# Performance work log

Measured on AMD Instinct MI355X. Metric: run time of the kernel, lower is better.

## Reference

```python
import jax, jax.numpy as jnp
import numpy as np

N_NODES = 50000


def gcn_conv(x, W, b, src, dst, num_nodes):
    """PyG GCNConv: add self-loops, symmetric deg^{-1/2} normalization,
    linear transform, scatter-add aggregation, bias."""
    loop = jnp.arange(num_nodes, dtype=src.dtype)
    s = jnp.concatenate([src, loop])  # message sources
    d = jnp.concatenate([dst, loop])  # message destinations
    deg = jax.ops.segment_sum(jnp.ones_like(d, dtype=x.dtype), d, num_segments=num_nodes)
    dinv = jnp.where(deg > 0, jax.lax.rsqrt(deg), 0.0)
    norm = dinv[s] * dinv[d]                      # [E+N]
    h = x @ W                                      # [N, out]
    msg = h[s] * norm[:, None]                     # gather + scale  [E+N, out]
    out = jax.ops.segment_sum(msg, d, num_segments=num_nodes)  # scatter-add
    return out + b


def setup_inputs() -> dict:
    key = jax.random.key(0)
    ks = jax.random.split(key, 8)
    n, e = N_NODES, 1600000
    d_in, d_h, d_out = 128, 128, 64
    x = jax.random.normal(ks[0], (n, d_in), dtype=jnp.float32)
    edge_index = jax.random.randint(ks[1], (2, e), 0, n, dtype=jnp.int32)
    s = 1.0 / np.sqrt(d_in)
    W1 = jax.random.uniform(ks[2], (d_in, d_h), jnp.float32, -s, s)
    b1 = jnp.zeros((d_h,), jnp.float32)
    W2 = jax.random.uniform(ks[3], (d_h, d_h), jnp.float32, -s, s)
    b2 = jnp.zeros((d_h,), jnp.float32)
    W3 = jax.random.uniform(ks[4], (d_h, d_out), jnp.float32, -s, s)
    b3 = jnp.zeros((d_out,), jnp.float32)
    return {"x": x, "edge_index": edge_index, "W1": W1, "b1": b1,
            "W2": W2, "b2": b2, "W3": W3, "b3": b3}


def reference(x, edge_index, W1, b1, W2, b2, W3, b3):
    src, dst = edge_index[0], edge_index[1]
    n = x.shape[0]
    # Dropout in eval mode (identity); ReLU between GCN layers.
    h = jax.nn.relu(gcn_conv(x, W1, b1, src, dst, n))
    h = jax.nn.relu(gcn_conv(h, W2, b2, src, dst, n))
    out = gcn_conv(h, W3, b3, src, dst, n)
    return out
```

## Files before the change

### kernel.cpp

```cpp
#include <hip/hip_runtime.h>
#include <type_traits>


#define EPB  4096
#define DIRW 197

typedef __attribute__((ext_vector_type(8))) short bf16x8;
typedef __attribute__((ext_vector_type(4))) float f32x4;
typedef __attribute__((ext_vector_type(2))) float f32x2;

__device__ __forceinline__ unsigned short f2bf(float f) {
    unsigned int u = __float_as_uint(f);
    u += 0x7FFFu + ((u >> 16) & 1u);
    return (unsigned short)(u >> 16);
}
__device__ __forceinline__ float bflo(unsigned int u) { return __uint_as_float(u << 16); }
__device__ __forceinline__ float bfhi(unsigned int u) { return __uint_as_float(u & 0xFFFF0000u); }

__global__ __launch_bounds__(256) void bin_wtrans_kernel(const int* __restrict__ src,
                                                         const int* __restrict__ dst,
                                                         unsigned int* __restrict__ pair_buf,
                                                         int* __restrict__ dir,
                                                         int E, int nbkt, int NB,
                                                         const float* __restrict__ W1,
                                                         const float* __restrict__ W2,
                                                         const float* __restrict__ W3,
                                                         unsigned short* __restrict__ Wt1,
                                                         unsigned short* __restrict__ Wt2,
                                                         unsigned short* __restrict__ Wt3,
                                                         unsigned int* __restrict__ hb_pad_row) {
    int blk = blockIdx.x;
    if (blk >= NB) {
        int wb = blk - NB;
        const float* W; unsigned short* Wt; int N, e0;
        if (wb < 64)       { W = W1; Wt = Wt1; N = 128; e0 = wb * 256; }
        else if (wb < 128) { W = W2; Wt = Wt2; N = 128; e0 = (wb - 64) * 256; }
        else               { W = W3; Wt = Wt3; N = 64;  e0 = (wb - 128) * 256; }
        int e = e0 + threadIdx.x;
        int nn = e >> 7, k = e & 127;
        Wt[e] = f2bf(W[(size_t)k * N + nn]);
        if (wb == 0 && threadIdx.x < 32) hb_pad_row[threadIdx.x] = 0u;
        return;
    }
    __shared__ unsigned int stage[EPB];
    __shared__ int hist[DIRW];
    __shared__ int sc[256];
    __shared__ int cur[DIRW];
    int tid = threadIdx.x;
    if (tid < DIRW) hist[tid] = 0;
    __syncthreads();

    int s_reg[16], d_reg[16];
#pragma unroll
    for (int j = 0; j < 16; ++j) {
        int gi = blk * EPB + j * 256 + tid;
        int s = 0, d = nbkt << 8;
        if (gi < E) { s = src[gi]; d = dst[gi]; }
        s_reg[j] = s; d_reg[j] = d;
        atomicAdd(&hist[d >> 8], 1);
    }
    __syncthreads();
    int h = (tid < DIRW) ? hist[tid] : 0;
    sc[tid] = h;
    __syncthreads();
#pragma unroll
    for (int off = 1; off < 256; off <<= 1) {
        int v = (tid >= off) ? sc[tid - off] : 0;
        __syncthreads();
        sc[tid] += v;
        __syncthreads();
    }
    if (tid < DIRW) {
        int st = sc[tid] - h;
        cur[tid] = st;
        dir[blk * DIRW + tid] = st;
    }
    __syncthreads();
#pragma unroll
    for (int j = 0; j < 16; ++j) {
        int b = d_reg[j] >> 8;
        int slot = atomicAdd(&cur[b], 1);
        stage[slot] = ((unsigned int)s_reg[j] << 8) | (unsigned int)(d_reg[j] & 255);
    }
    __syncthreads();
#pragma unroll
    for (int j = 0; j < 16; ++j) {
        int idx = j * 256 + tid;
        pair_buf[blk * EPB + idx] = stage[idx];
    }
}

__global__ __launch_bounds__(512) void csr_sizes_kernel(const unsigned int* __restrict__ pair_buf,
                                                        const int* __restrict__ dir,
                                                        int* __restrict__ bucket_pad,
                                                        int* __restrict__ node_cnt,
                                                        float* __restrict__ dinv,
                                                        int NB, int n) {
    __shared__ int dstart[400];
    __shared__ int dend[400];
    __shared__ int cnt[256];
    int tid = threadIdx.x;
    int b = blockIdx.x;
    for (int i = tid; i < NB; i += 512) {
        dstart[i] = dir[i * DIRW + b];
        dend[i]   = dir[i * DIRW + b + 1];
    }
    if (tid < 256) cnt[tid] = 0;
    __syncthreads();
    int wid = tid >> 6, lane = tid & 63;
    for (int seg = wid; seg < NB; seg += 8) {
        int s0 = dstart[seg], s1 = dend[seg];
        for (int k = s0 + lane; k < s1; k += 64) {
            unsigned int p = pair_buf[(size_t)seg * EPB + k];
            atomicAdd(&cnt[p & 255u], 1);
        }
    }
    __syncthreads();
    if (tid < 256) {
        node_cnt[b * 256 + tid] = cnt[tid];
        int d = b * 256 + tid;
        if (d < n) dinv[d] = rsqrtf((float)(cnt[tid] + 1));
    }
    if (tid < 64) {
        int m = max(max(cnt[4 * tid], cnt[4 * tid + 1]),
                    max(cnt[4 * tid + 2], cnt[4 * tid + 3]));
        int L = (m + 7) & ~7;
        int s = L;
#pragma unroll
        for (int off = 1; off < 64; off <<= 1) s += __shfl_xor(s, off);
        if (tid == 0) bucket_pad[b] = 4 * s;
    }
}

__global__ __launch_bounds__(512) void csr_place_kernel(const unsigned int* __restrict__ pair_buf,
                                                        const int* __restrict__ dir,
                                                        const int* __restrict__ bucket_pad,
                                                        const int* __restrict__ node_cnt,
                                                        int* __restrict__ row_ptr,
                                                        unsigned short* __restrict__ csr_src,
                                                        int n, int NB, int nbkt) {
    __shared__ int dstart[400];
    __shared__ int dend[400];
    __shared__ int psc[256];
    __shared__ int Lg[64];
    __shared__ int Lpre[64];
    __shared__ int nbase[256];
    __shared__ int cur[256];
    __shared__ int cend[256];
    int tid = threadIdx.x;
    int b = blockIdx.x;
    for (int i = tid; i < NB; i += 512) {
        dstart[i] = dir[i * DIRW + b];
        dend[i]   = dir[i * DIRW + b + 1];
    }
    if (tid < 256) psc[tid] = (tid < nbkt) ? bucket_pad[tid] : 0;
    __syncthreads();
#pragma unroll
    for (int off = 1; off < 256; off <<= 1) {
        int v = 0;
        if (tid < 256 && tid >= off) v = psc[tid - off];
        __syncthreads();
        if (tid < 256) psc[tid] += v;
        __syncthreads();
    }
    int base = (b > 0) ? psc[b - 1] : 0;
    if (b == nbkt - 1 && tid == 0) row_ptr[n] = psc[nbkt - 1];
    if (tid < 64) {
        int c0 = node_cnt[b * 256 + 4 * tid + 0];
        int c1 = node_cnt[b * 256 + 4 * tid + 1];
        int c2 = node_cnt[b * 256 + 4 * tid + 2];
        int c3 = node_cnt[b * 256 + 4 * tid + 3];
        int m = max(max(c0, c1), max(c2, c3));
        int L = (m + 7) & ~7;
        int x = L;
#pragma unroll
        for (int off = 1; off < 64; off <<= 1) {
            int y = __shfl_up(x, off);
            if (tid >= off) x += y;
        }
        Lg[tid] = L;
        Lpre[tid] = x - L;
    }
    __syncthreads();
    if (tid < 256) {
        int g = tid >> 2;
        int nb = base + 4 * Lpre[g] + (tid & 3) * Lg[g];
        nbase[tid] = nb;
        cur[tid] = nb;
        cend[tid] = nb + Lg[g];
        int d = b * 256 + tid;
        if (d < n) row_ptr[d] = nb;
    }
    __syncthreads();
    int wid = tid >> 6, lane = tid & 63;
    for (int seg = wid; seg < NB; seg += 8) {
        int s0 = dstart[seg], s1 = dend[seg];
        for (int k = s0 + lane; k < s1; k += 64) {
            unsigned int p = pair_buf[(size_t)seg * EPB + k];
            int pos = atomicAdd(&cur[p & 255u], 1);
            csr_src[pos] = (unsigned short)(p >> 8);
        }
    }
    __syncthreads();
    if (tid < 256) {
        for (int pos = cur[tid]; pos < cend[tid]; ++pos)
            csr_src[pos] = (unsigned short)n;
    }
}

template <int NOUT, typename TA, bool FP8OUT>
__global__ __launch_bounds__(256) void gemm_bf16_kernel(const TA* __restrict__ X,
                                                        const unsigned short* __restrict__ Wt,
                                                        const float* __restrict__ dinv,
                                                        void* __restrict__ Hout,
                                                        int n_rows) {
    __shared__ short As[64][136];
    __shared__ short Bs[NOUT][136];
    int tid = threadIdx.x;
    int row0 = blockIdx.x * 64;

    {
        int r = tid >> 2;
        int c0 = (tid & 3) * 32;
        int grow = row0 + r;
        if constexpr (std::is_same<TA, float>::value) {
            const float* xp = X + (size_t)grow * 128 + c0;
#pragma unroll
            for (int j = 0; j < 8; ++j) {
                float4 v = (grow < n_rows) ? *(const float4*)(xp + j * 4)
                                           : make_float4(0.f, 0.f, 0.f, 0.f);
                ushort4 p = { f2bf(v.x), f2bf(v.y), f2bf(v.z), f2bf(v.w) };
                *(ushort4*)&As[r][c0 + j * 4] = p;
            }
        } else {
            const unsigned short* xp = X + (size_t)grow * 128 + c0;
#pragma unroll
            for (int j = 0; j < 8; ++j) {
                uint2 v = (grow < n_rows) ? *(const uint2*)(xp + j * 4)
                                          : make_uint2(0u, 0u);
                *(uint2*)&As[r][c0 + j * 4] = v;
            }
        }
    }
    {
        constexpr int TPR = 256 / NOUT;
        constexpr int CH  = 128 / TPR;
        int nrow = tid / TPR;
        int seg  = tid % TPR;
        const unsigned short* wp = Wt + (size_t)nrow * 128 + seg * CH;
#pragma unroll
        for (int j = 0; j < CH / 8; ++j)
            *(uint4*)&Bs[nrow][seg * CH + j * 8] = *(const uint4*)(wp + j * 8);
    }
    __syncthreads();

    int w = tid >> 6, l = tid & 63, lr = l & 15, lg = l >> 4;
    constexpr int NF = NOUT / 16;
    f32x4 acc[NF];
#pragma unroll
    for (int i = 0; i < NF; ++i) acc[i] = (f32x4){0.f, 0.f, 0.f, 0.f};
    int arow = w * 16 + lr;

#pragma unroll
    for (int kc = 0; kc < 128; kc += 32) {
        bf16x8 a;
        ((long long*)&a)[0] = *(const long long*)&As[arow][kc + lg * 4];
        ((long long*)&a)[1] = *(const long long*)&As[arow][kc + 16 + lg * 4];
#pragma unroll
        for (int nf = 0; nf < NF; ++nf) {
            bf16x8 b;
            ((long long*)&b)[0] = *(const long long*)&Bs[nf * 16 + lr][kc + lg * 4];
            ((long long*)&b)[1] = *(const long long*)&Bs[nf * 16 + lr][kc + 16 + lg * 4];
            acc[nf] = __builtin_amdgcn_mfma_f32_16x16x32_bf16(a, b, acc[nf], 0, 0, 0);
        }
    }
    int grow_base = row0 + w * 16 + lg * 4;
    float dv[4];
#pragma unroll
    for (int r = 0; r < 4; ++r)
        dv[r] = (grow_base + r < n_rows) ? dinv[grow_base + r] : 0.f;
#pragma unroll
    for (int nf = 0; nf < NF; ++nf) {
#pragma unroll
        for (int r = 0; r < 4; ++r) {
            int gr = grow_base + r;
            if (gr < n_rows) {
                float val = acc[nf][r] * dv[r];
                if constexpr (FP8OUT) {
                    unsigned int pk = __builtin_amdgcn_cvt_pk_fp8_f32(val, val, 0, false);
                    ((unsigned char*)Hout)[(size_t)gr * NOUT + nf * 16 + lr] =
                        (unsigned char)(pk & 0xFFu);
                } else {
                    ((unsigned short*)Hout)[(size_t)gr * NOUT + nf * 16 + lr] = f2bf(val);
                }
            }
        }
    }
}

template <bool RELU>
__global__ __launch_bounds__(256) void agg128_kernel(const unsigned char* __restrict__ H,
                                                     const unsigned short* __restrict__ csr_src,
                                                     const int* __restrict__ row_ptr,
                                                     const float* __restrict__ dinv,
                                                     const float* __restrict__ bias,
                                                     unsigned short* __restrict__ out, int n) {
    int g = blockIdx.x * 4 + threadIdx.y;
    int node0 = g * 4;
    if (node0 >= n) return;
    int lane = threadIdx.x;
    int sub = lane >> 4, l16 = lane & 15;
    int node = node0 + sub;
    int base = row_ptr[node0];
    int L = (row_ptr[node0 + 4] - base) >> 2;
    int e0 = base + sub * L;
    const uint2* H2 = (const uint2*)H;
    float acc[8] = {0.f, 0.f, 0.f, 0.f, 0.f, 0.f, 0.f, 0.f};
    for (int k = 0; k < L; k += 8) {
        uint4 iv = *(const uint4*)(csr_src + e0 + k);
        int idx[8] = { (int)(iv.x & 0xFFFFu), (int)(iv.x >> 16),
                       (int)(iv.y & 0xFFFFu), (int)(iv.y >> 16),
                       (int)(iv.z & 0xFFFFu), (int)(iv.z >> 16),
                       (int)(iv.w & 0xFFFFu), (int)(iv.w >> 16) };
        uint2 v[8];
#pragma unroll
        for (int j = 0; j < 8; ++j) v[j] = H2[(size_t)idx[j] * 16 + l16];
#pragma unroll
        for (int j = 0; j < 8; ++j) {
            f32x2 a0 = __builtin_amdgcn_cvt_pk_f32_fp8((int)v[j].x, false);
            f32x2 a1 = __builtin_amdgcn_cvt_pk_f32_fp8((int)v[j].x, true);
            f32x2 a2 = __builtin_amdgcn_cvt_pk_f32_fp8((int)v[j].y, false);
            f32x2 a3 = __builtin_amdgcn_cvt_pk_f32_fp8((int)v[j].y, true);
            acc[0] += a0.x; acc[1] += a0.y; acc[2] += a1.x; acc[3] += a1.y;
            acc[4] += a2.x; acc[5] += a2.y; acc[6] += a3.x; acc[7] += a3.y;
        }
    }
    uint2 vn = H2[(size_t)node * 16 + l16];
    {
        f32x2 a0 = __builtin_amdgcn_cvt_pk_f32_fp8((int)vn.x, false);
        f32x2 a1 = __builtin_amdgcn_cvt_pk_f32_fp8((int)vn.x, true);
        f32x2 a2 = __builtin_amdgcn_cvt_pk_f32_fp8((int)vn.y, false);
        f32x2 a3 = __builtin_amdgcn_cvt_pk_f32_fp8((int)vn.y, true);
        acc[0] += a0.x; acc[1] += a0.y; acc[2] += a1.x; acc[3] += a1.y;
        acc[4] += a2.x; acc[5] += a2.y; acc[6] += a3.x; acc[7] += a3.y;
    }
    float dn = dinv[node];
    const float4* b4 = (const float4*)(bias + l16 * 8);
    float4 bb0 = b4[0], bb1 = b4[1];
    float r0 = fmaf(acc[0], dn, bb0.x), r1 = fmaf(acc[1], dn, bb0.y);
    float r2 = fmaf(acc[2], dn, bb0.z), r3 = fmaf(acc[3], dn, bb0.w);
    float r4 = fmaf(acc[4], dn, bb1.x), r5 = fmaf(acc[5], dn, bb1.y);
    float r6 = fmaf(acc[6], dn, bb1.z), r7 = fmaf(acc[7], dn, bb1.w);
    if (RELU) {
        r0 = fmaxf(r0, 0.f); r1 = fmaxf(r1, 0.f); r2 = fmaxf(r2, 0.f); r3 = fmaxf(r3, 0.f);
        r4 = fmaxf(r4, 0.f); r5 = fmaxf(r5, 0.f); r6 = fmaxf(r6, 0.f); r7 = fmaxf(r7, 0.f);
    }
    uint4 pk;
    pk.x = ((unsigned int)f2bf(r1) << 16) | (unsigned int)f2bf(r0);
    pk.y = ((unsigned int)f2bf(r3) << 16) | (unsigned int)f2bf(r2);
    pk.z = ((unsigned int)f2bf(r5) << 16) | (unsigned int)f2bf(r4);
    pk.w = ((unsigned int)f2bf(r7) << 16) | (unsigned int)f2bf(r6);
    ((uint4*)out)[(size_t)node * 16 + l16] = pk;
}

__global__ __launch_bounds__(256) void agg64_kernel(const unsigned short* __restrict__ H,
                                                    const unsigned short* __restrict__ csr_src,
                                                    const int* __restrict__ row_ptr,
                                                    const float* __restrict__ dinv,
                                                    const float* __restrict__ bias,
                                                    float* __restrict__ out, int n) {
    int g = blockIdx.x * 4 + threadIdx.y;
    int node0 = g * 4;
    if (node0 >= n) return;
    int lane = threadIdx.x;
    int sub = lane >> 4, l16 = lane & 15;
    int node = node0 + sub;
    int base = row_ptr[node0];
    int L = (row_ptr[node0 + 4] - base) >> 2;
    int e0 = base + sub * L;
    const uint2* H2 = (const uint2*)H;
    float acc[4] = {0.f, 0.f, 0.f, 0.f};
    for (int k = 0; k < L; k += 8) {
        uint4 iv = *(const uint4*)(csr_src + e0 + k);
        int idx[8] = { (int)(iv.x & 0xFFFFu), (int)(iv.x >> 16),
                       (int)(iv.y & 0xFFFFu), (int)(iv.y >> 16),
                       (int)(iv.z & 0xFFFFu), (int)(iv.z >> 16),
                       (int)(iv.w & 0xFFFFu), (int)(iv.w >> 16) };
        uint2 v[8];
#pragma unroll
        for (int j = 0; j < 8; ++j) v[j] = H2[(size_t)idx[j] * 16 + l16];
#pragma unroll
        for (int j = 0; j < 8; ++j) {
            acc[0] += bflo(v[j].x); acc[1] += bfhi(v[j].x);
            acc[2] += bflo(v[j].y); acc[3] += bfhi(v[j].y);
        }
    }
    uint2 vn = H2[(size_t)node * 16 + l16];
    acc[0] += bflo(vn.x); acc[1] += bfhi(vn.x);
    acc[2] += bflo(vn.y); acc[3] += bfhi(vn.y);
    float dn = dinv[node];
    float4 bb = *(const float4*)(bias + l16 * 4);
    float4 r;
    r.x = fmaf(acc[0], dn, bb.x);
    r.y = fmaf(acc[1], dn, bb.y);
    r.z = fmaf(acc[2], dn, bb.z);
    r.w = fmaf(acc[3], dn, bb.w);
    *(float4*)(out + (size_t)node * 64 + l16 * 4) = r;
}

extern "C" void kernel_launch(void* const* d_in, const int* in_sizes, int n_in,
                              void* d_out, int out_size, void* d_ws, size_t ws_size,
                              hipStream_t stream) {
    const float* x  = (const float*)d_in[0];
    const int*   ei = (const int*)d_in[1];
    const float* W1 = (const float*)d_in[2];
    const float* b1 = (const float*)d_in[3];
    const float* W2 = (const float*)d_in[4];
    const float* b2 = (const float*)d_in[5];
    const float* W3 = (const float*)d_in[6];
    const float* b3 = (const float*)d_in[7];

    const int n = in_sizes[0] / 128;
    const int E = in_sizes[1] / 2;
    const int* src = ei;
    const int* dst = ei + E;
    const int nbkt = (n + 255) >> 8;
    const int NB = (E + EPB - 1) / EPB;

    char* ws = (char*)d_ws;
    size_t off = 0;
    auto alloc = [&](size_t bytes) {
        void* p = ws + off;
        off = (off + bytes + 511) & ~(size_t)511;
        return p;
    };
    int*   bucket_pad  = (int*)alloc(256 * 4);
    int*   row_ptr     = (int*)alloc((size_t)(n + 1) * 4);
    float* dinv        = (float*)alloc((size_t)n * 4);
    int*   node_cnt    = (int*)alloc((size_t)nbkt * 256 * 4);
    unsigned short* csr_src = (unsigned short*)alloc((size_t)4000000 * 2);
    unsigned short* Wt1 = (unsigned short*)alloc(128 * 128 * 2);
    unsigned short* Wt2 = (unsigned short*)alloc(128 * 128 * 2);
    unsigned short* Wt3 = (unsigned short*)alloc(64 * 128 * 2);
    unsigned char* Hb  = (unsigned char*)alloc((size_t)(n + 1) * 128);
    unsigned short* Bb = (unsigned short*)alloc((size_t)n * 128 * 2);
    unsigned int* pair_buf = (unsigned int*)Bb;
    int*          dir      = (int*)((char*)Bb + (size_t)NB * EPB * 4);
    (void)ws_size;

    bin_wtrans_kernel<<<NB + 160, 256, 0, stream>>>(src, dst, pair_buf, dir, E, nbkt, NB,
                                                    W1, W2, W3, Wt1, Wt2, Wt3,
                                                    (unsigned int*)(Hb + (size_t)n * 128));
    csr_sizes_kernel<<<nbkt, 512, 0, stream>>>(pair_buf, dir, bucket_pad, node_cnt, dinv, NB, n);
    csr_place_kernel<<<nbkt, 512, 0, stream>>>(pair_buf, dir, bucket_pad, node_cnt,
                                               row_ptr, csr_src, n, NB, nbkt);

    dim3 aggBlock(64, 4);
    int aggGrid = (n / 4 + 3) / 4;
    int gemmGrid = (n + 63) / 64;

    gemm_bf16_kernel<128, float, true><<<gemmGrid, 256, 0, stream>>>(x, Wt1, dinv, Hb, n);
    agg128_kernel<true><<<aggGrid, aggBlock, 0, stream>>>(Hb, csr_src, row_ptr, dinv, b1, Bb, n);
    gemm_bf16_kernel<128, unsigned short, true><<<gemmGrid, 256, 0, stream>>>(Bb, Wt2, dinv, Hb, n);
    agg128_kernel<true><<<aggGrid, aggBlock, 0, stream>>>(Hb, csr_src, row_ptr, dinv, b2, Bb, n);
    gemm_bf16_kernel<64, unsigned short, false><<<gemmGrid, 256, 0, stream>>>(Bb, Wt3, dinv, Hb, n);
    agg64_kernel<<<aggGrid, aggBlock, 0, stream>>>((unsigned short*)Hb, csr_src, row_ptr,
                                                   dinv, b3, (float*)d_out, n);
}
```

Measured before the change: 189.1 us.

## Fuse aggregation with following layer's GEMM to skip bf16 intermediate round-trip

```diff
diff --git a/kernel.cpp b/kernel.cpp
--- a/kernel.cpp
+++ b/kernel.cpp
@@ -28,7 +28,8 @@
                                                          unsigned short* __restrict__ Wt1,
                                                          unsigned short* __restrict__ Wt2,
                                                          unsigned short* __restrict__ Wt3,
-                                                         unsigned int* __restrict__ hb_pad_row) {
+                                                         unsigned int* __restrict__ padA,
+                                                         unsigned int* __restrict__ padB) {
     int blk = blockIdx.x;
     if (blk >= NB) {
         int wb = blk - NB;
@@ -39,7 +40,10 @@
         int e = e0 + threadIdx.x;
         int nn = e >> 7, k = e & 127;
         Wt[e] = f2bf(W[(size_t)k * N + nn]);
-        if (wb == 0 && threadIdx.x < 32) hb_pad_row[threadIdx.x] = 0u;
+        if (wb == 0 && threadIdx.x < 32) {
+            padA[threadIdx.x] = 0u;
+            padB[threadIdx.x] = 0u;
+        }
         return;
     }
     __shared__ unsigned int stage[EPB];
@@ -208,39 +212,149 @@
     }
 }
 
-template <int NOUT, typename TA, bool FP8OUT>
-__global__ __launch_bounds__(256) void gemm_bf16_kernel(const TA* __restrict__ X,
-                                                        const unsigned short* __restrict__ Wt,
-                                                        const float* __restrict__ dinv,
-                                                        void* __restrict__ Hout,
-                                                        int n_rows) {
+__global__ __launch_bounds__(256) void gemm1_kernel(const float* __restrict__ X,
+                                                    const unsigned short* __restrict__ Wt,
+                                                    const float* __restrict__ dinv,
+                                                    unsigned char* __restrict__ Hout,
+                                                    int n_rows) {
     __shared__ short As[64][136];
-    __shared__ short Bs[NOUT][136];
+    __shared__ short Bs[128][136];
     int tid = threadIdx.x;
     int row0 = blockIdx.x * 64;
-
     {
         int r = tid >> 2;
         int c0 = (tid & 3) * 32;
         int grow = row0 + r;
-        if constexpr (std::is_same<TA, float>::value) {
-            const float* xp = X + (size_t)grow * 128 + c0;
-#pragma unroll
-            for (int j = 0; j < 8; ++j) {
-                float4 v = (grow < n_rows) ? *(const float4*)(xp + j * 4)
-                                           : make_float4(0.f, 0.f, 0.f, 0.f);
-                ushort4 p = { f2bf(v.x), f2bf(v.y), f2bf(v.z), f2bf(v.w) };
-                *(ushort4*)&As[r][c0 + j * 4] = p;
+        const float* xp = X + (size_t)grow * 128 + c0;
+#pragma unroll
+        for (int j = 0; j < 8; ++j) {
+            float4 v = (grow < n_rows) ? *(const float4*)(xp + j * 4)
+                                       : make_float4(0.f, 0.f, 0.f, 0.f);
+            ushort4 p = { f2bf(v.x), f2bf(v.y), f2bf(v.z), f2bf(v.w) };
+            *(ushort4*)&As[r][c0 + j * 4] = p;
+        }
+    }
+    {
+        int nrow = tid >> 1;
+        int seg = tid & 1;
+        const unsigned short* wp = Wt + (size_t)nrow * 128 + seg * 64;
+#pragma unroll
+        for (int j = 0; j < 8; ++j)
+            *(uint4*)&Bs[nrow][seg * 64 + j * 8] = *(const uint4*)(wp + j * 8);
+    }
+    __syncthreads();
+
+    int w = tid >> 6, l = tid & 63, lr = l & 15, lg = l >> 4;
+    f32x4 acc[8];
+#pragma unroll
+    for (int i = 0; i < 8; ++i) acc[i] = (f32x4){0.f, 0.f, 0.f, 0.f};
+    int arow = w * 16 + lr;
+#pragma unroll
+    for (int kc = 0; kc < 128; kc += 32) {
+        bf16x8 a;
+        ((long long*)&a)[0] = *(const long long*)&As[arow][kc + lg * 4];
+        ((long long*)&a)[1] = *(const long long*)&As[arow][kc + 16 + lg * 4];
+#pragma unroll
+        for (int nf = 0; nf < 8; ++nf) {
+            bf16x8 b;
+            ((long long*)&b)[0] = *(const long long*)&Bs[nf * 16 + lr][kc + lg * 4];
+            ((long long*)&b)[1] = *(const long long*)&Bs[nf * 16 + lr][kc + 16 + lg * 4];
+            acc[nf] = __builtin_amdgcn_mfma_f32_16x16x32_bf16(a, b, acc[nf], 0, 0, 0);
+        }
+    }
+    int grow_base = row0 + w * 16 + lg * 4;
+    float dv[4];
+#pragma unroll
+    for (int r = 0; r < 4; ++r)
+        dv[r] = (grow_base + r < n_rows) ? dinv[grow_base + r] : 0.f;
+#pragma unroll
+    for (int nf = 0; nf < 8; ++nf) {
+#pragma unroll
+        for (int r = 0; r < 4; ++r) {
+            int gr = grow_base + r;
+            if (gr < n_rows) {
+                float val = acc[nf][r] * dv[r];
+                unsigned int pk = __builtin_amdgcn_cvt_pk_fp8_f32(val, val, 0, false);
+                Hout[(size_t)gr * 128 + nf * 16 + lr] = (unsigned char)(pk & 0xFFu);
             }
-        } else {
-            const unsigned short* xp = X + (size_t)grow * 128 + c0;
-#pragma unroll
-            for (int j = 0; j < 8; ++j) {
-                uint2 v = (grow < n_rows) ? *(const uint2*)(xp + j * 4)
-                                          : make_uint2(0u, 0u);
-                *(uint2*)&As[r][c0 + j * 4] = v;
+        }
+    }
+}
+
+template <int NOUT, bool FP8OUT>
+__global__ __launch_bounds__(256) void fused_agg_gemm_kernel(
+        const unsigned char* __restrict__ H,
+        const unsigned short* __restrict__ csr_src,
+        const int* __restrict__ row_ptr,
+        const float* __restrict__ dinv,
+        const float* __restrict__ bias,
+        const unsigned short* __restrict__ Wt,
+        void* __restrict__ Hout, int n) {
+    __shared__ short As[64][136];
+    __shared__ short Bs[NOUT][136];
+    int tid = threadIdx.x;
+    int w = tid >> 6, l = tid & 63;
+    int sub = l >> 4, l16 = l & 15;
+    int blk_base = blockIdx.x * 64;
+    const uint2* H2 = (const uint2*)H;
+
+    for (int it = 0; it < 4; ++it) {
+        int node0 = blk_base + w * 16 + it * 4;
+        int node = node0 + sub;
+        float r0 = 0.f, r1 = 0.f, r2 = 0.f, r3 = 0.f,
+              r4 = 0.f, r5 = 0.f, r6 = 0.f, r7 = 0.f;
+        if (node0 < n) {
+            int base = row_ptr[node0];
+            int L = (row_ptr[node0 + 4] - base) >> 2;
+            int e0 = base + sub * L;
+            float acc[8] = {0.f, 0.f, 0.f, 0.f, 0.f, 0.f, 0.f, 0.f};
+            for (int k = 0; k < L; k += 8) {
+                uint4 iv = *(const uint4*)(csr_src + e0 + k);
+                int idx[8] = { (int)(iv.x & 0xFFFFu), (int)(iv.x >> 16),
+                               (int)(iv.y & 0xFFFFu), (int)(iv.y >> 16),
+                               (int)(iv.z & 0xFFFFu), (int)(iv.z >> 16),
+                               (int)(iv.w & 0xFFFFu), (int)(iv.w >> 16) };
+                uint2 v[8];
+#pragma unroll
+                for (int j = 0; j < 8; ++j) v[j] = H2[(size_t)idx[j] * 16 + l16];
+#pragma unroll
+                for (int j = 0; j < 8; ++j) {
+                    f32x2 a0 = __builtin_amdgcn_cvt_pk_f32_fp8((int)v[j].x, false);
+                    f32x2 a1 = __builtin_amdgcn_cvt_pk_f32_fp8((int)v[j].x, true);
+                    f32x2 a2 = __builtin_amdgcn_cvt_pk_f32_fp8((int)v[j].y, false);
+                    f32x2 a3 = __builtin_amdgcn_cvt_pk_f32_fp8((int)v[j].y, true);
+                    acc[0] += a0.x; acc[1] += a0.y; acc[2] += a1.x; acc[3] += a1.y;
+                    acc[4] += a2.x; acc[5] += a2.y; acc[6] += a3.x; acc[7] += a3.y;
+                }
             }
-        }
+            uint2 vn = H2[(size_t)node * 16 + l16];
+            {
+                f32x2 a0 = __builtin_amdgcn_cvt_pk_f32_fp8((int)vn.x, false);
+                f32x2 a1 = __builtin_amdgcn_cvt_pk_f32_fp8((int)vn.x, true);
+                f32x2 a2 = __builtin_amdgcn_cvt_pk_f32_fp8((int)vn.y, false);
+                f32x2 a3 = __builtin_amdgcn_cvt_pk_f32_fp8((int)vn.y, true);
+                acc[0] += a0.x; acc[1] += a0.y; acc[2] += a1.x; acc[3] += a1.y;
+                acc[4] += a2.x; acc[5] += a2.y; acc[6] += a3.x; acc[7] += a3.y;
+            }
+            float dn = dinv[node];
+            const float4* b4 = (const float4*)(bias + l16 * 8);
+            float4 bb0 = b4[0], bb1 = b4[1];
+            r0 = fmaxf(fmaf(acc[0], dn, bb0.x), 0.f);
+            r1 = fmaxf(fmaf(acc[1], dn, bb0.y), 0.f);
+            r2 = fmaxf(fmaf(acc[2], dn, bb0.z), 0.f);
+            r3 = fmaxf(fmaf(acc[3], dn, bb0.w), 0.f);
+            r4 = fmaxf(fmaf(acc[4], dn, bb1.x), 0.f);
+            r5 = fmaxf(fmaf(acc[5], dn, bb1.y), 0.f);
+            r6 = fmaxf(fmaf(acc[6], dn, bb1.z), 0.f);
+            r7 = fmaxf(fmaf(acc[7], dn, bb1.w), 0.f);
+        }
+        uint4 pk;
+        pk.x = ((unsigned int)f2bf(r1) << 16) | (unsigned int)f2bf(r0);
+        pk.y = ((unsigned int)f2bf(r3) << 16) | (unsigned int)f2bf(r2);
+        pk.z = ((unsigned int)f2bf(r5) << 16) | (unsigned int)f2bf(r4);
+        pk.w = ((unsigned int)f2bf(r7) << 16) | (unsigned int)f2bf(r6);
+        int lrow = w * 16 + it * 4 + sub;
+        *(uint4*)&As[lrow][l16 * 8] = pk;
     }
     {
         constexpr int TPR = 256 / NOUT;
@@ -253,114 +367,46 @@
             *(uint4*)&Bs[nrow][seg * CH + j * 8] = *(const uint4*)(wp + j * 8);
     }
     __syncthreads();
-
-    int w = tid >> 6, l = tid & 63, lr = l & 15, lg = l >> 4;
     constexpr int NF = NOUT / 16;
     f32x4 acc[NF];
 #pragma unroll
     for (int i = 0; i < NF; ++i) acc[i] = (f32x4){0.f, 0.f, 0.f, 0.f};
-    int arow = w * 16 + lr;
-
+    int arow = w * 16 + l16;
 #pragma unroll
     for (int kc = 0; kc < 128; kc += 32) {
         bf16x8 a;
-        ((long long*)&a)[0] = *(const long long*)&As[arow][kc + lg * 4];
-        ((long long*)&a)[1] = *(const long long*)&As[arow][kc + 16 + lg * 4];
+        ((long long*)&a)[0] = *(const long long*)&As[arow][kc + sub * 4];
+        ((long long*)&a)[1] = *(const long long*)&As[arow][kc + 16 + sub * 4];
 #pragma unroll
         for (int nf = 0; nf < NF; ++nf) {
             bf16x8 b;
-            ((long long*)&b)[0] = *(const long long*)&Bs[nf * 16 + lr][kc + lg * 4];
-            ((long long*)&b)[1] = *(const long long*)&Bs[nf * 16 + lr][kc + 16 + lg * 4];
+            ((long long*)&b)[0] = *(const long long*)&Bs[nf * 16 + l16][kc + sub * 4];
+            ((long long*)&b)[1] = *(const long long*)&Bs[nf * 16 + l16][kc + 16 + sub * 4];
             acc[nf] = __builtin_amdgcn_mfma_f32_16x16x32_bf16(a, b, acc[nf], 0, 0, 0);
         }
     }
-    int grow_base = row0 + w * 16 + lg * 4;
+    int grow_base = blk_base + w * 16 + sub * 4;
     float dv[4];
 #pragma unroll
     for (int r = 0; r < 4; ++r)
-        dv[r] = (grow_base + r < n_rows) ? dinv[grow_base + r] : 0.f;
+        dv[r] = (grow_base + r < n) ? dinv[grow_base + r] : 0.f;
 #pragma unroll
     for (int nf = 0; nf < NF; ++nf) {
 #pragma unroll
         for (int r = 0; r < 4; ++r) {
             int gr = grow_base + r;
-            if (gr < n_rows) {
+            if (gr < n) {
                 float val = acc[nf][r] * dv[r];
                 if constexpr (FP8OUT) {
                     unsigned int pk = __builtin_amdgcn_cvt_pk_fp8_f32(val, val, 0, false);
-                    ((unsigned char*)Hout)[(size_t)gr * NOUT + nf * 16 + lr] =
+                    ((unsigned char*)Hout)[(size_t)gr * NOUT + nf * 16 + l16] =
                         (unsigned char)(pk & 0xFFu);
                 } else {
-                    ((unsigned short*)Hout)[(size_t)gr * NOUT + nf * 16 + lr] = f2bf(val);
+                    ((unsigned short*)Hout)[(size_t)gr * NOUT + nf * 16 + l16] = f2bf(val);
                 }
             }
         }
     }
-}
-
-template <bool RELU>
-__global__ __launch_bounds__(256) void agg128_kernel(const unsigned char* __restrict__ H,
-                                                     const unsigned short* __restrict__ csr_src,
-                                                     const int* __restrict__ row_ptr,
-                                                     const float* __restrict__ dinv,
-                                                     const float* __restrict__ bias,
-                                                     unsigned short* __restrict__ out, int n) {
-    int g = blockIdx.x * 4 + threadIdx.y;
-    int node0 = g * 4;
-    if (node0 >= n) return;
-    int lane = threadIdx.x;
-    int sub = lane >> 4, l16 = lane & 15;
-    int node = node0 + sub;
-    int base = row_ptr[node0];
-    int L = (row_ptr[node0 + 4] - base) >> 2;
-    int e0 = base + sub * L;
-    const uint2* H2 = (const uint2*)H;
-    float acc[8] = {0.f, 0.f, 0.f, 0.f, 0.f, 0.f, 0.f, 0.f};
-    for (int k = 0; k < L; k += 8) {
-        uint4 iv = *(const uint4*)(csr_src + e0 + k);
-        int idx[8] = { (int)(iv.x & 0xFFFFu), (int)(iv.x >> 16),
-                       (int)(iv.y & 0xFFFFu), (int)(iv.y >> 16),
-                       (int)(iv.z & 0xFFFFu), (int)(iv.z >> 16),
-                       (int)(iv.w & 0xFFFFu), (int)(iv.w >> 16) };
-        uint2 v[8];
-#pragma unroll
-        for (int j = 0; j < 8; ++j) v[j] = H2[(size_t)idx[j] * 16 + l16];
-#pragma unroll
-        for (int j = 0; j < 8; ++j) {
-            f32x2 a0 = __builtin_amdgcn_cvt_pk_f32_fp8((int)v[j].x, false);
-            f32x2 a1 = __builtin_amdgcn_cvt_pk_f32_fp8((int)v[j].x, true);
-            f32x2 a2 = __builtin_amdgcn_cvt_pk_f32_fp8((int)v[j].y, false);
-            f32x2 a3 = __builtin_amdgcn_cvt_pk_f32_fp8((int)v[j].y, true);
-            acc[0] += a0.x; acc[1] += a0.y; acc[2] += a1.x; acc[3] += a1.y;
-            acc[4] += a2.x; acc[5] += a2.y; acc[6] += a3.x; acc[7] += a3.y;
-        }
-    }
-    uint2 vn = H2[(size_t)node * 16 + l16];
-    {
-        f32x2 a0 = __builtin_amdgcn_cvt_pk_f32_fp8((int)vn.x, false);
-        f32x2 a1 = __builtin_amdgcn_cvt_pk_f32_fp8((int)vn.x, true);
-        f32x2 a2 = __builtin_amdgcn_cvt_pk_f32_fp8((int)vn.y, false);
-        f32x2 a3 = __builtin_amdgcn_cvt_pk_f32_fp8((int)vn.y, true);
-        acc[0] += a0.x; acc[1] += a0.y; acc[2] += a1.x; acc[3] += a1.y;
-        acc[4] += a2.x; acc[5] += a2.y; acc[6] += a3.x; acc[7] += a3.y;
-    }
-    float dn = dinv[node];
-    const float4* b4 = (const float4*)(bias + l16 * 8);
-    float4 bb0 = b4[0], bb1 = b4[1];
-    float r0 = fmaf(acc[0], dn, bb0.x), r1 = fmaf(acc[1], dn, bb0.y);
-    float r2 = fmaf(acc[2], dn, bb0.z), r3 = fmaf(acc[3], dn, bb0.w);
-    float r4 = fmaf(acc[4], dn, bb1.x), r5 = fmaf(acc[5], dn, bb1.y);
-    float r6 = fmaf(acc[6], dn, bb1.z), r7 = fmaf(acc[7], dn, bb1.w);
-    if (RELU) {
-        r0 = fmaxf(r0, 0.f); r1 = fmaxf(r1, 0.f); r2 = fmaxf(r2, 0.f); r3 = fmaxf(r3, 0.f);
-        r4 = fmaxf(r4, 0.f); r5 = fmaxf(r5, 0.f); r6 = fmaxf(r6, 0.f); r7 = fmaxf(r7, 0.f);
-    }
-    uint4 pk;
-    pk.x = ((unsigned int)f2bf(r1) << 16) | (unsigned int)f2bf(r0);
-    pk.y = ((unsigned int)f2bf(r3) << 16) | (unsigned int)f2bf(r2);
-    pk.z = ((unsigned int)f2bf(r5) << 16) | (unsigned int)f2bf(r4);
-    pk.w = ((unsigned int)f2bf(r7) << 16) | (unsigned int)f2bf(r6);
-    ((uint4*)out)[(size_t)node * 16 + l16] = pk;
 }
 
 __global__ __launch_bounds__(256) void agg64_kernel(const unsigned short* __restrict__ H,
@@ -442,28 +488,29 @@
     unsigned short* Wt1 = (unsigned short*)alloc(128 * 128 * 2);
     unsigned short* Wt2 = (unsigned short*)alloc(128 * 128 * 2);
     unsigned short* Wt3 = (unsigned short*)alloc(64 * 128 * 2);
-    unsigned char* Hb  = (unsigned char*)alloc((size_t)(n + 1) * 128);
-    unsigned short* Bb = (unsigned short*)alloc((size_t)n * 128 * 2);
-    unsigned int* pair_buf = (unsigned int*)Bb;
-    int*          dir      = (int*)((char*)Bb + (size_t)NB * EPB * 4);
+    unsigned char* HA = (unsigned char*)alloc((size_t)(n + 1) * 128);
+    unsigned char* HB = (unsigned char*)alloc((size_t)(n + 1) * 128);
+    unsigned int* pair_buf = (unsigned int*)alloc((size_t)NB * EPB * 4);
+    int*          dir      = (int*)alloc((size_t)NB * DIRW * 4);
     (void)ws_size;
 
     bin_wtrans_kernel<<<NB + 160, 256, 0, stream>>>(src, dst, pair_buf, dir, E, nbkt, NB,
                                                     W1, W2, W3, Wt1, Wt2, Wt3,
-                                                    (unsigned int*)(Hb + (size_t)n * 128));
+                                                    (unsigned int*)(HA + (size_t)n * 128),
+                                                    (unsigned int*)(HB + (size_t)n * 128));
     csr_sizes_kernel<<<nbkt, 512, 0, stream>>>(pair_buf, dir, bucket_pad, node_cnt, dinv, NB, n);
     csr_place_kernel<<<nbkt, 512, 0, stream>>>(pair_buf, dir, bucket_pad, node_cnt,
                                                row_ptr, csr_src, n, NB, nbkt);
 
+    int gemmGrid = (n + 63) / 64;
+
+    gemm1_kernel<<<gemmGrid, 256, 0, stream>>>(x, Wt1, dinv, HA, n);
+    fused_agg_gemm_kernel<128, true><<<gemmGrid, 256, 0, stream>>>(
+        HA, csr_src, row_ptr, dinv, b1, Wt2, HB, n);
+    fused_agg_gemm_kernel<64, false><<<gemmGrid, 256, 0, stream>>>(
+        HB, csr_src, row_ptr, dinv, b2, Wt3, HA, n);
     dim3 aggBlock(64, 4);
     int aggGrid = (n / 4 + 3) / 4;
-    int gemmGrid = (n + 63) / 64;
-
-    gemm_bf16_kernel<128, float, true><<<gemmGrid, 256, 0, stream>>>(x, Wt1, dinv, Hb, n);
-    agg128_kernel<true><<<aggGrid, aggBlock, 0, stream>>>(Hb, csr_src, row_ptr, dinv, b1, Bb, n);
-    gemm_bf16_kernel<128, unsigned short, true><<<gemmGrid, 256, 0, stream>>>(Bb, Wt2, dinv, Hb, n);
-    agg128_kernel<true><<<aggGrid, aggBlock, 0, stream>>>(Hb, csr_src, row_ptr, dinv, b2, Bb, n);
-    gemm_bf16_kernel<64, unsigned short, false><<<gemmGrid, 256, 0, stream>>>(Bb, Wt3, dinv, Hb, n);
-    agg64_kernel<<<aggGrid, aggBlock, 0, stream>>>((unsigned short*)Hb, csr_src, row_ptr,
+    agg64_kernel<<<aggGrid, aggBlock, 0, stream>>>((unsigned short*)HA, csr_src, row_ptr,
                                                    dinv, b3, (float*)d_out, n);
 }
```

Result: slower. 193.1 us (+2.1%).
